# Optimization experiments

Hardware: AMD Instinct MI355X
Metric: run time of the kernel (lower is better)

## Reference

```python
import jax, jax.numpy as jnp
import numpy as np

N = 50000        # atoms
E = 1600000      # edges (precomputed radius graph)
H = 128          # hidden_channels
F = 64           # num_filters
G = 50           # num_gaussians
L = 3            # num_interactions
NG = 256         # graphs in batch
MAXZ = 100       # atomic-number vocabulary
CUTOFF = 10.0


def ssp(x):
    # ShiftedSoftplus
    return jax.nn.softplus(x) - jnp.log(2.0).astype(x.dtype)


def setup_inputs() -> dict:
    key = jax.random.key(0)
    ks = jax.random.split(key, 20)
    s = 0.1
    inp = {
        "z": jax.random.randint(ks[0], (N,), 0, MAXZ),
        "pos": jax.random.uniform(ks[1], (N, 3), dtype=jnp.float32) * 5.0,
        "batch": jnp.sort(jax.random.randint(ks[2], (N,), 0, NG)),
        "edge_index": jax.random.randint(ks[3], (2, E), 0, N),
        "emb": jax.random.normal(ks[4], (MAXZ, H), dtype=jnp.float32),
        # interaction-block params, stacked over L layers
        "mw1": jax.random.normal(ks[5], (L, G, F), dtype=jnp.float32) * s,
        "mb1": jnp.zeros((L, F), dtype=jnp.float32),
        "mw2": jax.random.normal(ks[6], (L, F, F), dtype=jnp.float32) * s,
        "mb2": jnp.zeros((L, F), dtype=jnp.float32),
        "l1w": jax.random.normal(ks[7], (L, H, F), dtype=jnp.float32) * s,  # no bias
        "l2w": jax.random.normal(ks[8], (L, F, H), dtype=jnp.float32) * s,
        "l2b": jnp.zeros((L, H), dtype=jnp.float32),
        "lw": jax.random.normal(ks[9], (L, H, H), dtype=jnp.float32) * s,
        "lb": jnp.zeros((L, H), dtype=jnp.float32),
        # output MLP
        "ow1": jax.random.normal(ks[10], (H, H // 2), dtype=jnp.float32) * s,
        "ob1": jnp.zeros((H // 2,), dtype=jnp.float32),
        "ow2": jax.random.normal(ks[11], (H // 2, 1), dtype=jnp.float32) * s,
        "ob2": jnp.zeros((1,), dtype=jnp.float32),
    }
    return inp


def reference(z, pos, batch, edge_index, emb, mw1, mb1, mw2, mb2,
              l1w, l2w, l2b, lw, lb, ow1, ob1, ow2, ob2):
    src = edge_index[0]  # j (message source)
    dst = edge_index[1]  # i (message target)

    h = emb[z]                                   # [N,H]

    # edge distances + Gaussian smearing
    d = jnp.linalg.norm(pos[src] - pos[dst], axis=-1)          # [E]
    offset = jnp.linspace(0.0, CUTOFF, G, dtype=jnp.float32)   # [G]
    coeff = -0.5 / (offset[1] - offset[0]) ** 2
    edge_attr = jnp.exp(coeff * (d[:, None] - offset) ** 2)    # [E,G]

    # cosine cutoff
    C = 0.5 * (jnp.cos(d * jnp.pi / CUTOFF) + 1.0)             # [E]

    for i in range(L):
        # per-edge filter MLP
        W = ssp(edge_attr @ mw1[i] + mb1[i]) @ mw2[i] + mb2[i]  # [E,F]
        W = W * C[:, None]
        xj = (h @ l1w[i])[src]                                  # gather [E,F]
        msg = xj * W                                            # [E,F]
        agg = jax.ops.segment_sum(msg, dst, num_segments=N)     # [N,F]
        x = agg @ l2w[i] + l2b[i]                               # [N,H]
        x = ssp(x)
        x = x @ lw[i] + lb[i]
        h = h + x                                               # residual

    # output network + per-graph sum readout
    h = ssp(h @ ow1 + ob1)
    h = h @ ow2 + ob2                                           # [N,1]
    out = jax.ops.segment_sum(h, batch, num_segments=NG)        # [NG,1]
    return out.squeeze(1)                                       # [NG]
```

## Files before the change

### kernel.cpp

```cpp
#include <hip/hip_runtime.h>


typedef short bf16x8 __attribute__((ext_vector_type(8)));
typedef unsigned short ushort8 __attribute__((ext_vector_type(8)));
typedef float floatx4 __attribute__((ext_vector_type(4)));

#define HCH 128
#define FCH 64
#define GCH 50
#define LN  3
#define TBL 4096
#define CAP2 12288
#define CHUNK 4096
#define DMAX 8.6603f

#define MFMA(a, b, c) __builtin_amdgcn_mfma_f32_16x16x32_bf16((a), (b), (c), 0, 0, 0)

__device__ __forceinline__ unsigned short f2bf(float x) {
    unsigned int u = __float_as_uint(x);
    unsigned int r = (u + 0x7FFFu + ((u >> 16) & 1u)) >> 16;
    return (unsigned short)r;
}

__device__ __forceinline__ unsigned pk2bf(float lo, float hi) {
    unsigned ulo = __float_as_uint(lo) + 0x8000u;
    unsigned uhi = __float_as_uint(hi) + 0x8000u;
    return __builtin_amdgcn_perm(uhi, ulo, 0x07060302u);
}

__device__ __forceinline__ float bf2f(unsigned short u) {
    return __uint_as_float((unsigned)u << 16);
}

__device__ __forceinline__ float sspf(float x) {
    float t = __expf(-fabsf(x));
    float l = __logf(1.f + t);
    return fmaxf(x, 0.f) + l - 0.69314718056f;
}

__device__ __forceinline__ void fill_frag(const float* __restrict__ src,
                                          short* __restrict__ dst,
                                          int K, int F, int Ksrc,
                                          int tid, int nthr)
{
    int kc = K >> 5;
    int total = (F >> 4) * kc * 512;
    for (int i = tid; i < total; i += nthr) {
        int j = i & 7;
        int lane = (i >> 3) & 63;
        int rest = i >> 9;
        int kk = rest % kc;
        int nt = rest / kc;
        int k = kk * 32 + ((lane >> 4) << 3) + j;
        int f = nt * 16 + (lane & 15);
        float v = (k < Ksrc) ? src[k * F + f] : 0.f;
        dst[i] = (short)f2bf(v);
    }
}

__global__ __launch_bounds__(64) void k_pre(
    const float* __restrict__ mw1, const float* __restrict__ mb1,
    const float* __restrict__ mw2, const float* __restrict__ mb2,
    unsigned short* __restrict__ Wtb,
    const float* __restrict__ l1w, const float* __restrict__ l2w,
    const float* __restrict__ lw,  const float* __restrict__ ow1,
    short* __restrict__ l1wp, short* __restrict__ l2wp,
    short* __restrict__ lwp,  short* __restrict__ ow1p,
    int* __restrict__ gcur, float* __restrict__ out, int nb2, int osz)
{
    __shared__ float sh[64];
    int blk = blockIdx.x;
    int f = threadIdx.x;
    if (blk < LN * TBL) {
        int l = blk / TBL, k = blk - l * TBL;
        float d = (float)k * (DMAX / (float)(TBL - 1));
        const float step = 10.f / 49.f;
        const float coeff = -0.5f / (step * step);
        float t1 = mb1[l * 64 + f];
        const float* w1 = mw1 + l * GCH * 64;
        for (int g = 0; g < GCH; g++) {
            float u = d - (float)g * step;
            t1 += __expf(coeff * u * u) * w1[g * 64 + f];
        }
        sh[f] = sspf(t1);
        float acc = mb2[l * 64 + f];
        const float* w2 = mw2 + l * 64 * 64;
        for (int g = 0; g < 64; g++) acc += sh[g] * w2[g * 64 + f];
        float C = 0.5f * (__cosf(d * 0.31415926535897932f) + 1.f);
        Wtb[(size_t)blk * 64 + f] = f2bf(acc * C);
    } else if (blk < LN * TBL + 32) {
        int tid = (blk - LN * TBL) * 64 + f;
        int nthr = 32 * 64;
        for (int l = 0; l < LN; l++) {
            fill_frag(l1w + l * HCH * FCH, l1wp + l * 8192, 128, 64, 128, tid, nthr);
            fill_frag(l2w + l * FCH * HCH, l2wp + l * 8192, 64, 128, 64, tid, nthr);
            fill_frag(lw  + l * HCH * HCH, lwp  + l * 16384, 128, 128, 128, tid, nthr);
        }
        fill_frag(ow1, ow1p, 128, 64, 128, tid, nthr);
    } else {
        for (int i = f; i < nb2 * 16; i += 64) gcur[i] = 0;
        for (int i = f; i < osz; i += 64) out[i] = 0.f;
    }
}

__global__ __launch_bounds__(256) void k_s1(
    const int* __restrict__ ei, const float* __restrict__ pos,
    int* __restrict__ gcur, int2* __restrict__ ebuf, int E, int nb2)
{
    __shared__ int hist[256];
    __shared__ int lstart[256];
    __shared__ int lcur[256];
    __shared__ int gbase[256];
    __shared__ int wsum[4];
    __shared__ int2 stage[CHUNK];

    int t = threadIdx.x, lane = t & 63, w = t >> 6;
    int e0 = blockIdx.x * CHUNK;
    int e1 = min(e0 + CHUNK, E);
    int cnt = e1 - e0;

    hist[t] = 0;
    __syncthreads();

    int2 my[16];
    int  mybk[16];
#pragma unroll
    for (int i = 0; i < 16; i++) {
        int e = e0 + t + i * 256;
        int ec = min(e, E - 1);
        int s = ei[ec];
        int d2 = ei[E + ec];
        float dx = pos[s * 3 + 0] - pos[d2 * 3 + 0];
        float dy = pos[s * 3 + 1] - pos[d2 * 3 + 1];
        float dz = pos[s * 3 + 2] - pos[d2 * 3 + 2];
        float dist = sqrtf(dx * dx + dy * dy + dz * dz);
        int tix = (int)(dist * ((float)(TBL - 1) / DMAX) + 0.5f);
        tix = (tix > TBL - 1) ? (TBL - 1) : tix;
        my[i] = make_int2(s | (tix << 17), d2);
        mybk[i] = (e < e1) ? (d2 >> 8) : -1;
        if (mybk[i] >= 0) atomicAdd(&hist[mybk[i]], 1);
    }
    __syncthreads();

    int base0;
    {
        int c = hist[t];
        int a = c;
#pragma unroll
        for (int o = 1; o < 64; o <<= 1) {
            int u = __shfl_up(a, o, 64);
            if (lane >= o) a += u;
        }
        if (lane == 63) wsum[w] = a;
        __syncthreads();
        int prefix = 0;
#pragma unroll
        for (int i = 0; i < 4; i++) if (i < w) prefix += wsum[i];
        int ls = prefix + a - c;
        lstart[t] = ls; lcur[t] = ls;
        base0 = (c && t < nb2) ? atomicAdd(&gcur[t * 16], c) : 0;
    }
    __syncthreads();

#pragma unroll
    for (int i = 0; i < 16; i++) {
        if (mybk[i] >= 0) {
            int ofs = atomicAdd(&lcur[mybk[i]], 1);
            stage[ofs] = my[i];
        }
    }
    gbase[t] = t * CAP2 + base0;
    __syncthreads();

    for (int i = t; i < cnt; i += 256) {
        int2 ed = stage[i];
        int bk = ed.y >> 8;
        int g = gbase[bk] + (i - lstart[bk]);
        if (g < bk * CAP2 + CAP2) ebuf[g] = ed;
    }
}

__global__ __launch_bounds__(512) void k_s2n0(
    const int2* __restrict__ ebuf, const int* __restrict__ gcur,
    int2* __restrict__ edata, int* __restrict__ rowptr, int nb2,
    const int* __restrict__ z, const float* __restrict__ emb,
    const short* __restrict__ l1wp0, float* __restrict__ h,
    unsigned short* __restrict__ xjb, int N)
{
    __shared__ int hist[256];
    __shared__ int bcur[256];
    __shared__ int wred[8];
    __shared__ __align__(16) short A3[8192];
    __shared__ int zL[64];
    int t = threadIdx.x, lane = t & 63, w = t >> 6;
    int bk = blockIdx.x;
    if (bk < nb2) {
        int cnt = min(gcur[bk * 16], CAP2);
        int v = (t < bk && t < nb2) ? min(gcur[t * 16], CAP2) : 0;
#pragma unroll
        for (int o = 32; o; o >>= 1) v += __shfl_down(v, o, 64);
        if (lane == 0) wred[w] = v;
        if (t < 256) hist[t] = 0;
        __syncthreads();
        int gs = 0;
#pragma unroll
        for (int i = 0; i < 8; i++) gs += wred[i];

        const int2* eb = ebuf + (size_t)bk * CAP2;
        for (int i = t; i < cnt; i += 512)
            atomicAdd(&hist[eb[i].y & 255], 1);
        __syncthreads();
        int myc = (t < 256) ? hist[t] : 0;
        for (int o = 1; o < 256; o <<= 1) {
            int u = (t < 256 && t >= o) ? hist[t - o] : 0;
            __syncthreads();
            if (t < 256) hist[t] += u;
            __syncthreads();
        }
        if (t < 256) {
            int start = gs + hist[t] - myc;
            bcur[t] = start;
            rowptr[(bk << 8) + t] = start;
        }
        if (bk == nb2 - 1 && t == 0) rowptr[nb2 << 8] = gs + cnt;
        __syncthreads();
        for (int i = t; i < cnt; i += 512) {
            int2 ed = eb[i];
            int dl = ed.y & 255;
            int p = atomicAdd(&bcur[dl], 1);
            edata[p] = ed;
        }
    } else {
        int n0 = (bk - nb2) * 64;
        if (t < 64) { int n = n0 + t; zL[t] = (n < N) ? z[n] : 0; }
        __syncthreads();
        if (t < 256) {
#pragma unroll
            for (int m = 0; m < 16; m++) {
                int ii = lane + 64 * m;
                int rloc = ii >> 6;
                int k0 = (ii & 63) * 2;
                int n = n0 + w * 16 + rloc;
                float2 v = make_float2(0.f, 0.f);
                if (n < N) {
                    v = *(const float2*)(&emb[(size_t)zL[w * 16 + rloc] * HCH + k0]);
                    *(float2*)(&h[(size_t)n * HCH + k0]) = v;
                }
                unsigned pk = pk2bf(v.x, v.y);
                int si = w * 2048 + (k0 >> 5) * 512 + (rloc + 16 * ((k0 >> 3) & 3)) * 8 + (k0 & 7);
                *(unsigned*)(&A3[si]) = pk;
            }
            int quad = lane >> 4, col = lane & 15;
            const bf16x8* B = (const bf16x8*)l1wp0;
            bf16x8 af[4];
#pragma unroll
            for (int kk = 0; kk < 4; kk++)
                af[kk] = *(const bf16x8*)(&A3[w * 2048 + kk * 512 + lane * 8]);
#pragma unroll
            for (int nt = 0; nt < 4; nt++) {
                floatx4 c = {0.f, 0.f, 0.f, 0.f};
#pragma unroll
                for (int kk = 0; kk < 4; kk++) c = MFMA(af[kk], B[(nt * 4 + kk) * 64 + lane], c);
                int f = nt * 16 + col;
#pragma unroll
                for (int reg = 0; reg < 4; reg++) {
                    int n = n0 + w * 16 + quad * 4 + reg;
                    if (n < N) xjb[(size_t)n * FCH + f] = f2bf(c[reg]);
                }
            }
        }
    }
}

__global__ __launch_bounds__(256) void k_edge(
    const int* __restrict__ rowptr, const int2* __restrict__ edata,
    const unsigned short* __restrict__ xjb, const unsigned short* __restrict__ Wt,
    unsigned short* __restrict__ aggb, int N)
{
    int t = threadIdx.x, lane = t & 63, w = t >> 6;
    int n = blockIdx.x * 4 + w;
    if (n >= N) return;
    int beg = rowptr[n];
    int end = rowptr[n + 1];
    int slot = lane >> 3;
    int cq = (lane & 7) * 8;
    const unsigned short* xp = xjb + cq;
    const unsigned short* wp = Wt + cq;
    float acc[8];
#pragma unroll
    for (int j = 0; j < 8; j++) acc[j] = 0.f;
    for (int e = beg; e < end; e += 16) {
        int eb = e + slot * 2;
        int2 ed0 = edata[min(eb + 0, end - 1)];
        int2 ed1 = edata[min(eb + 1, end - 1)];
        int exv[2] = {ed0.x, ed1.x};
        uint4 xq[2], wq[2];
#pragma unroll
        for (int i = 0; i < 2; i++) {
            int s   = exv[i] & 0x1FFFF;
            int tix = (int)(((unsigned)exv[i]) >> 17);
            xq[i] = *(const uint4*)(xp + ((size_t)s << 6));
            wq[i] = *(const uint4*)(wp + ((size_t)tix << 6));
        }
#pragma unroll
        for (int i = 0; i < 2; i++) {
            if (eb + i >= end) { wq[i].x = 0u; wq[i].y = 0u; wq[i].z = 0u; wq[i].w = 0u; }
            acc[0] += __uint_as_float(xq[i].x << 16)         * __uint_as_float(wq[i].x << 16);
            acc[1] += __uint_as_float(xq[i].x & 0xFFFF0000u) * __uint_as_float(wq[i].x & 0xFFFF0000u);
            acc[2] += __uint_as_float(xq[i].y << 16)         * __uint_as_float(wq[i].y << 16);
            acc[3] += __uint_as_float(xq[i].y & 0xFFFF0000u) * __uint_as_float(wq[i].y & 0xFFFF0000u);
            acc[4] += __uint_as_float(xq[i].z << 16)         * __uint_as_float(wq[i].z << 16);
            acc[5] += __uint_as_float(xq[i].z & 0xFFFF0000u) * __uint_as_float(wq[i].z & 0xFFFF0000u);
            acc[6] += __uint_as_float(xq[i].w << 16)         * __uint_as_float(wq[i].w << 16);
            acc[7] += __uint_as_float(xq[i].w & 0xFFFF0000u) * __uint_as_float(wq[i].w & 0xFFFF0000u);
        }
    }
#pragma unroll
    for (int o = 8; o < 64; o <<= 1) {
#pragma unroll
        for (int j = 0; j < 8; j++) acc[j] += __shfl_xor(acc[j], o, 64);
    }
    if (slot == 0) {
        uint4 pk;
        pk.x = pk2bf(acc[0], acc[1]);
        pk.y = pk2bf(acc[2], acc[3]);
        pk.z = pk2bf(acc[4], acc[5]);
        pk.w = pk2bf(acc[6], acc[7]);
        *(uint4*)(aggb + (size_t)n * FCH + cq) = pk;
    }
}

__global__ __launch_bounds__(256) void k_update(
    const unsigned short* __restrict__ aggb, const short* __restrict__ l2wp,
    const float* __restrict__ l2b, const short* __restrict__ lwp,
    const float* __restrict__ lb,  const short* __restrict__ l1wp_next,
    float* __restrict__ h, unsigned short* __restrict__ xjb, int layer, int N)
{
    __shared__ __align__(16) short AR[8192];
    int t = threadIdx.x, lane = t & 63, w = t >> 6;
    int n0 = blockIdx.x * 64;
    short* WR = &AR[w * 2048];
#pragma unroll
    for (int m = 0; m < 8; m++) {
        int ii = lane + 64 * m;
        int rloc = ii >> 5;
        int k0 = (ii & 31) * 2;
        int n = n0 + w * 16 + rloc;
        unsigned pk = 0u;
        if (n < N) pk = *(const unsigned*)(&aggb[(size_t)n * FCH + k0]);
        int si = (k0 >> 5) * 512 + (rloc + 16 * ((k0 >> 3) & 3)) * 8 + (k0 & 7);
        *(unsigned*)(&WR[si]) = pk;
    }
    int quad = lane >> 4, col = lane & 15;
    const bf16x8* Bl2 = (const bf16x8*)(l2wp + layer * 8192);
    const bf16x8* Blw = (const bf16x8*)(lwp + layer * 16384);
    const bf16x8* Bl1 = (const bf16x8*)l1wp_next;

    bf16x8 a0 = *(const bf16x8*)(&WR[lane * 8]);
    bf16x8 a1 = *(const bf16x8*)(&WR[512 + lane * 8]);
#pragma unroll
    for (int nt = 0; nt < 8; nt++) {
        float bias = l2b[layer * HCH + nt * 16 + col];
        floatx4 c = {bias, bias, bias, bias};
        c = MFMA(a0, Bl2[(nt * 2 + 0) * 64 + lane], c);
        c = MFMA(a1, Bl2[(nt * 2 + 1) * 64 + lane], c);
        int f = nt * 16 + col;
        int si0 = (f >> 5) * 512 + (16 * ((f >> 3) & 3)) * 8 + (f & 7);
#pragma unroll
        for (int reg = 0; reg < 4; reg++)
            WR[si0 + (quad * 4 + reg) * 8] = (short)f2bf(sspf(c[reg]));
    }
    bf16x8 af[4];
#pragma unroll
    for (int kk = 0; kk < 4; kk++)
        af[kk] = *(const bf16x8*)(&WR[kk * 512 + lane * 8]);
#pragma unroll
    for (int nt = 0; nt < 8; nt++) {
        float bias = lb[layer * HCH + nt * 16 + col];
        floatx4 c = {bias, bias, bias, bias};
#pragma unroll
        for (int kk = 0; kk < 4; kk++) c = MFMA(af[kk], Blw[(nt * 4 + kk) * 64 + lane], c);
        int f = nt * 16 + col;
        int si0 = (f >> 5) * 512 + (16 * ((f >> 3) & 3)) * 8 + (f & 7);
#pragma unroll
        for (int reg = 0; reg < 4; reg++) {
            int n = n0 + w * 16 + quad * 4 + reg;
            float hv = 0.f;
            if (n < N) {
                hv = h[(size_t)n * HCH + f] + c[reg];
                h[(size_t)n * HCH + f] = hv;
            }
            WR[si0 + (quad * 4 + reg) * 8] = (short)f2bf(hv);
        }
    }
#pragma unroll
    for (int kk = 0; kk < 4; kk++)
        af[kk] = *(const bf16x8*)(&WR[kk * 512 + lane * 8]);
#pragma unroll
    for (int nt = 0; nt < 4; nt++) {
        floatx4 c = {0.f, 0.f, 0.f, 0.f};
#pragma unroll
        for (int kk = 0; kk < 4; kk++) c = MFMA(af[kk], Bl1[(nt * 4 + kk) * 64 + lane], c);
        int f = nt * 16 + col;
#pragma unroll
        for (int reg = 0; reg < 4; reg++) {
            int n = n0 + w * 16 + quad * 4 + reg;
            if (n < N) xjb[(size_t)n * FCH + f] = f2bf(c[reg]);
        }
    }
}

__global__ __launch_bounds__(256) void k_final(
    const unsigned short* __restrict__ aggb, const short* __restrict__ l2wp,
    const float* __restrict__ l2b, const short* __restrict__ lwp,
    const float* __restrict__ lb,  const short* __restrict__ ow1p,
    const float* __restrict__ ob1, const float* __restrict__ ow2,
    const float* __restrict__ ob2, const int* __restrict__ batch,
    const float* __restrict__ h, float* __restrict__ out, int layer, int N)
{
    __shared__ __align__(16) short AR[8192];
    __shared__ float R[64 * 17];
    int t = threadIdx.x, lane = t & 63, w = t >> 6;
    int n0 = blockIdx.x * 64;
    short* WR = &AR[w * 2048];
#pragma unroll
    for (int m = 0; m < 8; m++) {
        int ii = lane + 64 * m;
        int rloc = ii >> 5;
        int k0 = (ii & 31) * 2;
        int n = n0 + w * 16 + rloc;
        unsigned pk = 0u;
        if (n < N) pk = *(const unsigned*)(&aggb[(size_t)n * FCH + k0]);
        int si = (k0 >> 5) * 512 + (rloc + 16 * ((k0 >> 3) & 3)) * 8 + (k0 & 7);
        *(unsigned*)(&WR[si]) = pk;
    }
    int quad = lane >> 4, col = lane & 15;
    const bf16x8* Bl2 = (const bf16x8*)(l2wp + layer * 8192);
    const bf16x8* Blw = (const bf16x8*)(lwp + layer * 16384);
    const bf16x8* Bow = (const bf16x8*)ow1p;

    bf16x8 a0 = *(const bf16x8*)(&WR[lane * 8]);
    bf16x8 a1 = *(const bf16x8*)(&WR[512 + lane * 8]);
#pragma unroll
    for (int nt = 0; nt < 8; nt++) {
        float bias = l2b[layer * HCH + nt * 16 + col];
        floatx4 c = {bias, bias, bias, bias};
        c = MFMA(a0, Bl2[(nt * 2 + 0) * 64 + lane], c);
        c = MFMA(a1, Bl2[(nt * 2 + 1) * 64 + lane], c);
        int f = nt * 16 + col;
        int si0 = (f >> 5) * 512 + (16 * ((f >> 3) & 3)) * 8 + (f & 7);
#pragma unroll
        for (int reg = 0; reg < 4; reg++)
            WR[si0 + (quad * 4 + reg) * 8] = (short)f2bf(sspf(c[reg]));
    }
    bf16x8 af[4];
#pragma unroll
    for (int kk = 0; kk < 4; kk++)
        af[kk] = *(const bf16x8*)(&WR[kk * 512 + lane * 8]);
#pragma unroll
    for (int nt = 0; nt < 8; nt++) {
        float bias = lb[layer * HCH + nt * 16 + col];
        floatx4 c = {bias, bias, bias, bias};
#pragma unroll
        for (int kk = 0; kk < 4; kk++) c = MFMA(af[kk], Blw[(nt * 4 + kk) * 64 + lane], c);
        int f = nt * 16 + col;
        int si0 = (f >> 5) * 512 + (16 * ((f >> 3) & 3)) * 8 + (f & 7);
#pragma unroll
        for (int reg = 0; reg < 4; reg++) {
            int n = n0 + w * 16 + quad * 4 + reg;
            float hv = 0.f;
            if (n < N) hv = h[(size_t)n * HCH + f] + c[reg];
            WR[si0 + (quad * 4 + reg) * 8] = (short)f2bf(hv);
        }
    }
#pragma unroll
    for (int kk = 0; kk < 4; kk++)
        af[kk] = *(const bf16x8*)(&WR[kk * 512 + lane * 8]);
    float p[4] = {0.f, 0.f, 0.f, 0.f};
#pragma unroll
    for (int nt = 0; nt < 4; nt++) {
        float bias = ob1[nt * 16 + col];
        floatx4 c = {bias, bias, bias, bias};
#pragma unroll
        for (int kk = 0; kk < 4; kk++) c = MFMA(af[kk], Bow[(nt * 4 + kk) * 64 + lane], c);
        float w2 = ow2[nt * 16 + col];
#pragma unroll
        for (int reg = 0; reg < 4; reg++) p[reg] += sspf(c[reg]) * w2;
    }
#pragma unroll
    for (int reg = 0; reg < 4; reg++)
        R[(w * 16 + quad * 4 + reg) * 17 + col] = p[reg];
    __syncthreads();
    if (t < 64) {
        int n = n0 + t;
        float v = 0.f;
        int g = -1;
        if (n < N) {
            v = ob2[0];
#pragma unroll
            for (int c2 = 0; c2 < 16; c2++) v += R[t * 17 + c2];
            g = batch[n];
        }
#pragma unroll
        for (int off2 = 1; off2 < 64; off2 <<= 1) {
            float vv = __shfl_down(v, off2, 64);
            int gg = __shfl_down(g, off2, 64);
            if (lane + off2 < 64 && gg == g) v += vv;
        }
        int gp = __shfl_up(g, 1, 64);
        bool head = (lane == 0) || (g != gp);
        if (head && g >= 0) unsafeAtomicAdd(&out[g], v);
    }
}

extern "C" void kernel_launch(void* const* d_in, const int* in_sizes, int n_in,
                              void* d_out, int out_size, void* d_ws, size_t ws_size,
                              hipStream_t stream)
{
    const int*   z    = (const int*)d_in[0];
    const float* pos  = (const float*)d_in[1];
    const int*   batc = (const int*)d_in[2];
    const int*   ei   = (const int*)d_in[3];
    const float* emb  = (const float*)d_in[4];
    const float* mw1  = (const float*)d_in[5];
    const float* mb1  = (const float*)d_in[6];
    const float* mw2  = (const float*)d_in[7];
    const float* mb2  = (const float*)d_in[8];
    const float* l1w  = (const float*)d_in[9];
    const float* l2w  = (const float*)d_in[10];
    const float* l2b  = (const float*)d_in[11];
    const float* lw   = (const float*)d_in[12];
    const float* lb   = (const float*)d_in[13];
    const float* ow1  = (const float*)d_in[14];
    const float* ob1  = (const float*)d_in[15];
    const float* ow2  = (const float*)d_in[16];
    const float* ob2  = (const float*)d_in[17];
    float* out = (float*)d_out;

    int N = in_sizes[0];
    int E = in_sizes[3] / 2;
    int nb2 = (N + 255) >> 8;

    char* ws = (char*)d_ws;
    size_t off = 0;
    auto alloc = [&](size_t bytes) {
        void* p = ws + off;
        off = (off + bytes + 255) & ~(size_t)255;
        return p;
    };
    float* h      = (float*)alloc((size_t)N * HCH * 4);
    unsigned short* xjb = (unsigned short*)alloc((size_t)N * FCH * 2);
    unsigned short* aggb = (unsigned short*)alloc((size_t)N * FCH * 2);
    int2*  ebuf   = (int2*)alloc((size_t)nb2 * CAP2 * 8);
    int2*  edata  = (int2*)alloc((size_t)E * 8);
    unsigned short* Wtab = (unsigned short*)alloc((size_t)LN * TBL * 64 * 2);
    int*   gcur   = (int*)alloc((size_t)nb2 * 64);
    int*   rowptr = (int*)alloc(((size_t)nb2 * 256 + 1) * 4);
    short* l1wp   = (short*)alloc(LN * 8192 * 2);
    short* l2wp   = (short*)alloc(LN * 8192 * 2);
    short* lwp    = (short*)alloc(LN * 16384 * 2);
    short* ow1p   = (short*)alloc(8192 * 2);

    int NB = (N + 63) / 64;
    int NB4 = (N + 3) / 4;
    int S1B = (E + CHUNK - 1) / CHUNK;
    int PREB = LN * TBL + 32 + 1;

    k_pre<<<PREB, 64, 0, stream>>>(mw1, mb1, mw2, mb2, Wtab,
                                   l1w, l2w, lw, ow1, l1wp, l2wp, lwp, ow1p,
                                   gcur, out, nb2, out_size);
    k_s1<<<S1B, 256, 0, stream>>>(ei, pos, gcur, ebuf, E, nb2);
    k_s2n0<<<nb2 + NB, 512, 0, stream>>>(ebuf, gcur, edata, rowptr, nb2,
                                         z, emb, l1wp, h, xjb, N);
    for (int l = 0; l < LN; l++) {
        k_edge<<<NB4, 256, 0, stream>>>(rowptr, edata, xjb,
                                        Wtab + (size_t)l * TBL * 64, aggb, N);
        if (l < LN - 1) {
            k_update<<<NB, 256, 0, stream>>>(aggb, l2wp, l2b, lwp, lb,
                                             l1wp + (l + 1) * 8192, h, xjb, l, N);
        } else {
            k_final<<<NB, 256, 0, stream>>>(aggb, l2wp, l2b, lwp, lb, ow1p,
                                            ob1, ow2, ob2, batc, h, out, 2, N);
        }
    }
}
```

Baseline: 330.4 us.

## Fuse table precompute with edge bucketing and store only packed edge source index

Merges the filter-table/weight-packing kernel and the edge-bucketing kernel into one launch, so independent setup work runs concurrently instead of in two serialized launches. The table build now uses 256-thread blocks computing four distances each and shuffles instead of shared memory. The gcur reset moves to a hipMemsetAsync, and the sorted edge array stores only the packed src/tix int instead of an int2, halving index traffic in the three edge passes. The added memset launch and the larger shared-memory footprint of the fused kernel's table blocks may lower occupancy for that part.

New measurement: 320.5 us. 1.03x faster.

```diff
diff --git a/kernel.cpp b/kernel.cpp
--- a/kernel.cpp
+++ b/kernel.cpp
@@ -58,7 +58,8 @@
     }
 }
 
-__global__ __launch_bounds__(64) void k_pre(
+#define WTB (LN * TBL / 4)
+__global__ __launch_bounds__(256) void k_ps1(
     const float* __restrict__ mw1, const float* __restrict__ mb1,
     const float* __restrict__ mw2, const float* __restrict__ mb2,
     unsigned short* __restrict__ Wtb,
@@ -66,13 +67,24 @@
     const float* __restrict__ lw,  const float* __restrict__ ow1,
     short* __restrict__ l1wp, short* __restrict__ l2wp,
     short* __restrict__ lwp,  short* __restrict__ ow1p,
-    int* __restrict__ gcur, float* __restrict__ out, int nb2, int osz)
-{
-    __shared__ float sh[64];
+    float* __restrict__ out, int osz,
+    const int* __restrict__ ei, const float* __restrict__ pos,
+    int* __restrict__ gcur, int2* __restrict__ ebuf, int E, int nb2)
+{
+    __shared__ int hist[256];
+    __shared__ int lstart[256];
+    __shared__ int lcur[256];
+    __shared__ int gbase[256];
+    __shared__ int wsum[4];
+    __shared__ int2 stage[CHUNK];
+
     int blk = blockIdx.x;
-    int f = threadIdx.x;
-    if (blk < LN * TBL) {
-        int l = blk / TBL, k = blk - l * TBL;
+    int t = threadIdx.x, lane = t & 63, w = t >> 6;
+
+    if (blk < WTB) {
+        int idx = blk * 4 + w;
+        int l = idx / TBL, k = idx - l * TBL;
+        int f = lane;
         float d = (float)k * (DMAX / (float)(TBL - 1));
         const float step = 10.f / 49.f;
         const float coeff = -0.5f / (step * step);
@@ -82,107 +94,93 @@
             float u = d - (float)g * step;
             t1 += __expf(coeff * u * u) * w1[g * 64 + f];
         }
-        sh[f] = sspf(t1);
+        float sv = sspf(t1);
         float acc = mb2[l * 64 + f];
         const float* w2 = mw2 + l * 64 * 64;
-        for (int g = 0; g < 64; g++) acc += sh[g] * w2[g * 64 + f];
+        for (int g = 0; g < 64; g++) acc += __shfl(sv, g, 64) * w2[g * 64 + f];
         float C = 0.5f * (__cosf(d * 0.31415926535897932f) + 1.f);
-        Wtb[(size_t)blk * 64 + f] = f2bf(acc * C);
-    } else if (blk < LN * TBL + 32) {
-        int tid = (blk - LN * TBL) * 64 + f;
-        int nthr = 32 * 64;
+        Wtb[(size_t)idx * 64 + f] = f2bf(acc * C);
+    } else if (blk < WTB + 32) {
+        int tid = (blk - WTB) * 256 + t;
+        int nthr = 32 * 256;
         for (int l = 0; l < LN; l++) {
             fill_frag(l1w + l * HCH * FCH, l1wp + l * 8192, 128, 64, 128, tid, nthr);
             fill_frag(l2w + l * FCH * HCH, l2wp + l * 8192, 64, 128, 64, tid, nthr);
             fill_frag(lw  + l * HCH * HCH, lwp  + l * 16384, 128, 128, 128, tid, nthr);
         }
         fill_frag(ow1, ow1p, 128, 64, 128, tid, nthr);
+    } else if (blk == WTB + 32) {
+        for (int i = t; i < osz; i += 256) out[i] = 0.f;
     } else {
-        for (int i = f; i < nb2 * 16; i += 64) gcur[i] = 0;
-        for (int i = f; i < osz; i += 64) out[i] = 0.f;
-    }
-}
-
-__global__ __launch_bounds__(256) void k_s1(
-    const int* __restrict__ ei, const float* __restrict__ pos,
-    int* __restrict__ gcur, int2* __restrict__ ebuf, int E, int nb2)
-{
-    __shared__ int hist[256];
-    __shared__ int lstart[256];
-    __shared__ int lcur[256];
-    __shared__ int gbase[256];
-    __shared__ int wsum[4];
-    __shared__ int2 stage[CHUNK];
-
-    int t = threadIdx.x, lane = t & 63, w = t >> 6;
-    int e0 = blockIdx.x * CHUNK;
-    int e1 = min(e0 + CHUNK, E);
-    int cnt = e1 - e0;
-
-    hist[t] = 0;
-    __syncthreads();
-
-    int2 my[16];
-    int  mybk[16];
-#pragma unroll
-    for (int i = 0; i < 16; i++) {
-        int e = e0 + t + i * 256;
-        int ec = min(e, E - 1);
-        int s = ei[ec];
-        int d2 = ei[E + ec];
-        float dx = pos[s * 3 + 0] - pos[d2 * 3 + 0];
-        float dy = pos[s * 3 + 1] - pos[d2 * 3 + 1];
-        float dz = pos[s * 3 + 2] - pos[d2 * 3 + 2];
-        float dist = sqrtf(dx * dx + dy * dy + dz * dz);
-        int tix = (int)(dist * ((float)(TBL - 1) / DMAX) + 0.5f);
-        tix = (tix > TBL - 1) ? (TBL - 1) : tix;
-        my[i] = make_int2(s | (tix << 17), d2);
-        mybk[i] = (e < e1) ? (d2 >> 8) : -1;
-        if (mybk[i] >= 0) atomicAdd(&hist[mybk[i]], 1);
-    }
-    __syncthreads();
-
-    int base0;
-    {
-        int c = hist[t];
-        int a = c;
-#pragma unroll
-        for (int o = 1; o < 64; o <<= 1) {
-            int u = __shfl_up(a, o, 64);
-            if (lane >= o) a += u;
-        }
-        if (lane == 63) wsum[w] = a;
-        __syncthreads();
-        int prefix = 0;
-#pragma unroll
-        for (int i = 0; i < 4; i++) if (i < w) prefix += wsum[i];
-        int ls = prefix + a - c;
-        lstart[t] = ls; lcur[t] = ls;
-        base0 = (c && t < nb2) ? atomicAdd(&gcur[t * 16], c) : 0;
-    }
-    __syncthreads();
-
-#pragma unroll
-    for (int i = 0; i < 16; i++) {
-        if (mybk[i] >= 0) {
-            int ofs = atomicAdd(&lcur[mybk[i]], 1);
-            stage[ofs] = my[i];
-        }
-    }
-    gbase[t] = t * CAP2 + base0;
-    __syncthreads();
-
-    for (int i = t; i < cnt; i += 256) {
-        int2 ed = stage[i];
-        int bk = ed.y >> 8;
-        int g = gbase[bk] + (i - lstart[bk]);
-        if (g < bk * CAP2 + CAP2) ebuf[g] = ed;
+        int e0 = (blk - WTB - 33) * CHUNK;
+        int e1 = min(e0 + CHUNK, E);
+        int cnt = e1 - e0;
+
+        hist[t] = 0;
+        __syncthreads();
+
+        int2 my[16];
+        int  mybk[16];
+#pragma unroll
+        for (int i = 0; i < 16; i++) {
+            int e = e0 + t + i * 256;
+            int ec = min(e, E - 1);
+            int s = ei[ec];
+            int d2 = ei[E + ec];
+            float dx = pos[s * 3 + 0] - pos[d2 * 3 + 0];
+            float dy = pos[s * 3 + 1] - pos[d2 * 3 + 1];
+            float dz = pos[s * 3 + 2] - pos[d2 * 3 + 2];
+            float dist = sqrtf(dx * dx + dy * dy + dz * dz);
+            int tix = (int)(dist * ((float)(TBL - 1) / DMAX) + 0.5f);
+            tix = (tix > TBL - 1) ? (TBL - 1) : tix;
+            my[i] = make_int2(s | (tix << 17), d2);
+            mybk[i] = (e < e1) ? (d2 >> 8) : -1;
+            if (mybk[i] >= 0) atomicAdd(&hist[mybk[i]], 1);
+        }
+        __syncthreads();
+
+        int base0;
+        {
+            int c = hist[t];
+            int a = c;
+#pragma unroll
+            for (int o = 1; o < 64; o <<= 1) {
+                int u = __shfl_up(a, o, 64);
+                if (lane >= o) a += u;
+            }
+            if (lane == 63) wsum[w] = a;
+            __syncthreads();
+            int prefix = 0;
+#pragma unroll
+            for (int i = 0; i < 4; i++) if (i < w) prefix += wsum[i];
+            int ls = prefix + a - c;
+            lstart[t] = ls; lcur[t] = ls;
+            base0 = (c && t < nb2) ? atomicAdd(&gcur[t * 16], c) : 0;
+        }
+        __syncthreads();
+
+#pragma unroll
+        for (int i = 0; i < 16; i++) {
+            if (mybk[i] >= 0) {
+                int ofs = atomicAdd(&lcur[mybk[i]], 1);
+                stage[ofs] = my[i];
+            }
+        }
+        gbase[t] = t * CAP2 + base0;
+        __syncthreads();
+
+        for (int i = t; i < cnt; i += 256) {
+            int2 ed = stage[i];
+            int bk = ed.y >> 8;
+            int g = gbase[bk] + (i - lstart[bk]);
+            if (g < bk * CAP2 + CAP2) ebuf[g] = ed;
+        }
     }
 }
 
 __global__ __launch_bounds__(512) void k_s2n0(
     const int2* __restrict__ ebuf, const int* __restrict__ gcur,
-    int2* __restrict__ edata, int* __restrict__ rowptr, int nb2,
+    int* __restrict__ edx, int* __restrict__ rowptr, int nb2,
     const int* __restrict__ z, const float* __restrict__ emb,
     const short* __restrict__ l1wp0, float* __restrict__ h,
     unsigned short* __restrict__ xjb, int N)
@@ -228,7 +226,7 @@
             int2 ed = eb[i];
             int dl = ed.y & 255;
             int p = atomicAdd(&bcur[dl], 1);
-            edata[p] = ed;
+            edx[p] = ed.x;
         }
     } else {
         int n0 = (bk - nb2) * 64;
@@ -273,7 +271,7 @@
 }
 
 __global__ __launch_bounds__(256) void k_edge(
-    const int* __restrict__ rowptr, const int2* __restrict__ edata,
+    const int* __restrict__ rowptr, const int* __restrict__ edx,
     const unsigned short* __restrict__ xjb, const unsigned short* __restrict__ Wt,
     unsigned short* __restrict__ aggb, int N)
 {
@@ -291,9 +289,9 @@
     for (int j = 0; j < 8; j++) acc[j] = 0.f;
     for (int e = beg; e < end; e += 16) {
         int eb = e + slot * 2;
-        int2 ed0 = edata[min(eb + 0, end - 1)];
-        int2 ed1 = edata[min(eb + 1, end - 1)];
-        int exv[2] = {ed0.x, ed1.x};
+        int exv[2];
+        exv[0] = edx[min(eb + 0, end - 1)];
+        exv[1] = edx[min(eb + 1, end - 1)];
         uint4 xq[2], wq[2];
 #pragma unroll
         for (int i = 0; i < 2; i++) {
@@ -552,7 +550,7 @@
     unsigned short* xjb = (unsigned short*)alloc((size_t)N * FCH * 2);
     unsigned short* aggb = (unsigned short*)alloc((size_t)N * FCH * 2);
     int2*  ebuf   = (int2*)alloc((size_t)nb2 * CAP2 * 8);
-    int2*  edata  = (int2*)alloc((size_t)E * 8);
+    int*   edx    = (int*)alloc((size_t)E * 4);
     unsigned short* Wtab = (unsigned short*)alloc((size_t)LN * TBL * 64 * 2);
     int*   gcur   = (int*)alloc((size_t)nb2 * 64);
     int*   rowptr = (int*)alloc(((size_t)nb2 * 256 + 1) * 4);
@@ -564,16 +562,17 @@
     int NB = (N + 63) / 64;
     int NB4 = (N + 3) / 4;
     int S1B = (E + CHUNK - 1) / CHUNK;
-    int PREB = LN * TBL + 32 + 1;
-
-    k_pre<<<PREB, 64, 0, stream>>>(mw1, mb1, mw2, mb2, Wtab,
-                                   l1w, l2w, lw, ow1, l1wp, l2wp, lwp, ow1p,
-                                   gcur, out, nb2, out_size);
-    k_s1<<<S1B, 256, 0, stream>>>(ei, pos, gcur, ebuf, E, nb2);
-    k_s2n0<<<nb2 + NB, 512, 0, stream>>>(ebuf, gcur, edata, rowptr, nb2,
+    int PS1B = WTB + 32 + 1 + S1B;
+
+    hipMemsetAsync(gcur, 0, (size_t)nb2 * 64, stream);
+    k_ps1<<<PS1B, 256, 0, stream>>>(mw1, mb1, mw2, mb2, Wtab,
+                                    l1w, l2w, lw, ow1, l1wp, l2wp, lwp, ow1p,
+                                    out, out_size,
+                                    ei, pos, gcur, ebuf, E, nb2);
+    k_s2n0<<<nb2 + NB, 512, 0, stream>>>(ebuf, gcur, edx, rowptr, nb2,
                                          z, emb, l1wp, h, xjb, N);
     for (int l = 0; l < LN; l++) {
-        k_edge<<<NB4, 256, 0, stream>>>(rowptr, edata, xjb,
+        k_edge<<<NB4, 256, 0, stream>>>(rowptr, edx, xjb,
                                         Wtab + (size_t)l * TBL * 64, aggb, N);
         if (l < LN - 1) {
             k_update<<<NB, 256, 0, stream>>>(aggb, l2wp, l2b, lwp, lb,
```
